# Kernel optimization log

Measured on AMD Instinct MI355X. Metric: run time of the kernel, lower is better.

Reference implementation:

```python
import jax, jax.numpy as jnp
import numpy as np

VOCAB, DIM, B, L, OUT = 100000, 50, 4096, 512, 20

def setup_inputs() -> dict:
    key = jax.random.key(0)
    k1, k2, k3, k4, k5 = jax.random.split(key, 5)
    x = jax.random.randint(k1, (B, L), 0, VOCAB, dtype=jnp.int64)
    lengths = jax.random.randint(k2, (B,), 1, L + 1, dtype=jnp.int64)  # at least 1 token
    emb_table = jax.random.normal(k3, (VOCAB, DIM), dtype=jnp.float32)
    W = jax.random.normal(k4, (OUT, DIM), dtype=jnp.float32) * 0.1
    b = jax.random.normal(k5, (OUT,), dtype=jnp.float32) * 0.1
    return {"x": x, "lengths": lengths, "emb_table": emb_table, "W": W, "b": b}

def reference(x, lengths, emb_table, W, b):
    # embedding gather: [B, L, D]
    emb = emb_table[x]
    # masked mean over the first lengths[i] tokens of each sample
    mask = (jnp.arange(emb.shape[1])[None, :] < lengths[:, None]).astype(emb.dtype)  # [B, L]
    denom = lengths.astype(emb.dtype)[:, None]                                        # [B, 1]
    rep = jnp.einsum('bld,bl->bd', emb, mask) / denom                                 # [B, D]
    rep = jax.nn.relu(rep)
    logits = rep @ W.T + b                                                            # [B, OUT]
    return logits
```

## Files before the change

kernel.cpp:

```cpp
#include <hip/hip_runtime.h>
#include <hip/hip_fp16.h>


#define LMAX    512
#define DIMV    50
#define OUTV    20
#define VOCABSZ 100000
#define RSTRIDE 64

struct __align__(16) H8 { __half2 h[4]; };

__global__ __launch_bounds__(256) void build_tab(
    const float* __restrict__ emb, __half* __restrict__ tab)
{
    const int t = blockIdx.x * 256 + threadIdx.x;
    const int r = t >> 3;
    const int q = t & 7;
    if (r > VOCABSZ) return;
    float v[8] = {0.f, 0.f, 0.f, 0.f, 0.f, 0.f, 0.f, 0.f};
    if (r < VOCABSZ) {
        const float* src = emb + r * DIMV + q * 8;
        if (q < 6) {
            #pragma unroll
            for (int j = 0; j < 8; j += 2) {
                float2 a = *reinterpret_cast<const float2*>(src + j);
                v[j] = a.x; v[j + 1] = a.y;
            }
        } else if (q == 6) {
            float2 a = *reinterpret_cast<const float2*>(src);
            v[0] = a.x; v[1] = a.y;
        }
    }
    H8 h;
    h.h[0] = __floats2half2_rn(v[0], v[1]);
    h.h[1] = __floats2half2_rn(v[2], v[3]);
    h.h[2] = __floats2half2_rn(v[4], v[5]);
    h.h[3] = __floats2half2_rn(v[6], v[7]);
    *reinterpret_cast<H8*>(tab + r * RSTRIDE + q * 8) = h;
}

__device__ inline void accum(float4& a0, float4& a1, const H8& h) {
    float2 f0 = __half22float2(h.h[0]);
    float2 f1 = __half22float2(h.h[1]);
    float2 f2 = __half22float2(h.h[2]);
    float2 f3 = __half22float2(h.h[3]);
    a0.x += f0.x; a0.y += f0.y; a0.z += f1.x; a0.w += f1.y;
    a1.x += f2.x; a1.y += f2.y; a1.z += f3.x; a1.w += f3.y;
}

__global__ __launch_bounds__(256) void fused_gather(
    const int*    __restrict__ x,
    const int*    __restrict__ lengths,
    const __half* __restrict__ tab,
    const float*  __restrict__ W,
    const float*  __restrict__ bias,
    float*        __restrict__ out)
{
    const int b    = blockIdx.x;
    const int tid  = threadIdx.x;
    const int wave = tid >> 6;
    const int lane = tid & 63;
    const int rg   = lane >> 3;
    const int cl   = lane & 7;

    __shared__ int   sidx[LMAX];
    __shared__ float sacc[4][64];
    __shared__ float srep[DIMV];

    const int len = lengths[b];

    const int xbase = b * LMAX;
    #pragma unroll
    for (int i = 0; i < LMAX; i += 256) {
        const int ii = i + tid;
        const int v  = x[xbase + ii];
        sidx[ii] = (ii < len) ? v : VOCABSZ;
    }
    __syncthreads();

    const __half* tabc = tab + cl * 8;
    const int nchunk = (len + 7) >> 3;
    float4 a0 = {0.f, 0.f, 0.f, 0.f};
    float4 a1 = {0.f, 0.f, 0.f, 0.f};

    int c = wave;
    for (; c + 28 < nchunk; c += 32) {
        int i0 = sidx[(c     ) * 8 + rg];
        int i1 = sidx[(c +  4) * 8 + rg];
        int i2 = sidx[(c +  8) * 8 + rg];
        int i3 = sidx[(c + 12) * 8 + rg];
        int i4 = sidx[(c + 16) * 8 + rg];
        int i5 = sidx[(c + 20) * 8 + rg];
        int i6 = sidx[(c + 24) * 8 + rg];
        int i7 = sidx[(c + 28) * 8 + rg];
        H8 h0 = *reinterpret_cast<const H8*>(tabc + (i0 << 6));
        H8 h1 = *reinterpret_cast<const H8*>(tabc + (i1 << 6));
        H8 h2 = *reinterpret_cast<const H8*>(tabc + (i2 << 6));
        H8 h3 = *reinterpret_cast<const H8*>(tabc + (i3 << 6));
        H8 h4 = *reinterpret_cast<const H8*>(tabc + (i4 << 6));
        H8 h5 = *reinterpret_cast<const H8*>(tabc + (i5 << 6));
        H8 h6 = *reinterpret_cast<const H8*>(tabc + (i6 << 6));
        H8 h7 = *reinterpret_cast<const H8*>(tabc + (i7 << 6));
        accum(a0, a1, h0); accum(a0, a1, h1); accum(a0, a1, h2); accum(a0, a1, h3);
        accum(a0, a1, h4); accum(a0, a1, h5); accum(a0, a1, h6); accum(a0, a1, h7);
    }
    for (; c < nchunk; c += 4) {
        int i0 = sidx[c * 8 + rg];
        H8 h0 = *reinterpret_cast<const H8*>(tabc + (i0 << 6));
        accum(a0, a1, h0);
    }

    #pragma unroll
    for (int m = 8; m <= 32; m <<= 1) {
        a0.x += __shfl_xor(a0.x, m); a0.y += __shfl_xor(a0.y, m);
        a0.z += __shfl_xor(a0.z, m); a0.w += __shfl_xor(a0.w, m);
        a1.x += __shfl_xor(a1.x, m); a1.y += __shfl_xor(a1.y, m);
        a1.z += __shfl_xor(a1.z, m); a1.w += __shfl_xor(a1.w, m);
    }
    if (lane < 8) {
        *reinterpret_cast<float4*>(&sacc[wave][lane * 8])     = a0;
        *reinterpret_cast<float4*>(&sacc[wave][lane * 8 + 4]) = a1;
    }
    __syncthreads();

    if (tid < DIMV) {
        float s = sacc[0][tid] + sacc[1][tid] + sacc[2][tid] + sacc[3][tid];
        srep[tid] = fmaxf(s / (float)len, 0.f);
    }
    __syncthreads();

    if (tid < OUTV) {
        float s = bias[tid];
        const float* wr = W + tid * DIMV;
        #pragma unroll
        for (int d = 0; d < DIMV; ++d) s += srep[d] * wr[d];
        out[b * OUTV + tid] = s;
    }
}

extern "C" void kernel_launch(void* const* d_in, const int* in_sizes, int n_in,
                              void* d_out, int out_size, void* d_ws, size_t ws_size,
                              hipStream_t stream) {
    const int*   x       = (const int*)  d_in[0];
    const int*   lengths = (const int*)  d_in[1];
    const float* emb     = (const float*)d_in[2];
    const float* W       = (const float*)d_in[3];
    const float* bias    = (const float*)d_in[4];
    float*  out = (float*)d_out;
    __half* tab = (__half*)d_ws;

    const int B = in_sizes[1];

    const int nthr = (VOCABSZ + 1) * 8;
    build_tab<<<(nthr + 255) / 256, 256, 0, stream>>>(emb, tab);
    fused_gather<<<B, 256, 0, stream>>>(x, lengths, tab, W, bias, out);
}
```

Measured before the change: 97.61 us.

## Bin token indices by vocab shard and gather per shard for cache locality

Merges table conversion with a per-sample binning pass that groups valid token indices into 8 vocabulary shards, padded to multiples of 8. A shard-major gather kernel then makes concurrently running blocks touch the same ~1.6MB slice of the half table, aiming to raise L2 hit rate, and writes per-shard partial sums. A finalize kernel reduces the partials and applies mean, ReLU and the linear layer. This adds an extra pass over the indices, workspace round trips and two more launches, and concurrently running blocks may not actually stay within one shard.

```diff
diff --git a/kernel.cpp b/kernel.cpp
--- a/kernel.cpp
+++ b/kernel.cpp
@@ -7,37 +7,16 @@
 #define OUTV    20
 #define VOCABSZ 100000
 #define RSTRIDE 64
+#define NSHARD  8
+#define SHROWS  12500
+#define BINCAP  576
+#define TABBLKS 3126
 
 struct __align__(16) H8 { __half2 h[4]; };
 
-__global__ __launch_bounds__(256) void build_tab(
-    const float* __restrict__ emb, __half* __restrict__ tab)
-{
-    const int t = blockIdx.x * 256 + threadIdx.x;
-    const int r = t >> 3;
-    const int q = t & 7;
-    if (r > VOCABSZ) return;
-    float v[8] = {0.f, 0.f, 0.f, 0.f, 0.f, 0.f, 0.f, 0.f};
-    if (r < VOCABSZ) {
-        const float* src = emb + r * DIMV + q * 8;
-        if (q < 6) {
-            #pragma unroll
-            for (int j = 0; j < 8; j += 2) {
-                float2 a = *reinterpret_cast<const float2*>(src + j);
-                v[j] = a.x; v[j + 1] = a.y;
-            }
-        } else if (q == 6) {
-            float2 a = *reinterpret_cast<const float2*>(src);
-            v[0] = a.x; v[1] = a.y;
-        }
-    }
-    H8 h;
-    h.h[0] = __floats2half2_rn(v[0], v[1]);
-    h.h[1] = __floats2half2_rn(v[2], v[3]);
-    h.h[2] = __floats2half2_rn(v[4], v[5]);
-    h.h[3] = __floats2half2_rn(v[6], v[7]);
-    *reinterpret_cast<H8*>(tab + r * RSTRIDE + q * 8) = h;
-}
+#define OFF_GBIN  (16u << 20)
+#define OFF_BOFS  (28u << 20)
+#define OFF_PART  (29u << 20)
 
 __device__ inline void accum(float4& a0, float4& a1, const H8& h) {
     float2 f0 = __half22float2(h.h[0]);
@@ -46,6 +25,174 @@
     float2 f3 = __half22float2(h.h[3]);
     a0.x += f0.x; a0.y += f0.y; a0.z += f1.x; a0.w += f1.y;
     a1.x += f2.x; a1.y += f2.y; a1.z += f3.x; a1.w += f3.y;
+}
+
+__global__ __launch_bounds__(256) void prep(
+    const float* __restrict__ emb, const int* __restrict__ x,
+    const int* __restrict__ lengths, char* __restrict__ ws)
+{
+    const int tid = threadIdx.x;
+
+    if (blockIdx.x < TABBLKS) {
+        __half* tab = (__half*)ws;
+        const int t = blockIdx.x * 256 + tid;
+        const int r = t >> 3, q = t & 7;
+        if (r > VOCABSZ) return;
+        float v[8] = {0.f,0.f,0.f,0.f,0.f,0.f,0.f,0.f};
+        if (r < VOCABSZ) {
+            const float* src = emb + r * DIMV + q * 8;
+            if (q < 6) {
+                #pragma unroll
+                for (int j = 0; j < 8; j += 2) {
+                    float2 a = *reinterpret_cast<const float2*>(src + j);
+                    v[j] = a.x; v[j + 1] = a.y;
+                }
+            } else if (q == 6) {
+                float2 a = *reinterpret_cast<const float2*>(src);
+                v[0] = a.x; v[1] = a.y;
+            }
+        }
+        H8 h;
+        h.h[0] = __floats2half2_rn(v[0], v[1]);
+        h.h[1] = __floats2half2_rn(v[2], v[3]);
+        h.h[2] = __floats2half2_rn(v[4], v[5]);
+        h.h[3] = __floats2half2_rn(v[6], v[7]);
+        *reinterpret_cast<H8*>(tab + r * RSTRIDE + q * 8) = h;
+        return;
+    }
+
+    const int b = blockIdx.x - TABBLKS;
+    int*  gbin = (int*)(ws + OFF_GBIN);
+    int2* bofs = (int2*)(ws + OFF_BOFS);
+
+    __shared__ int sidx[LMAX];
+    __shared__ int sbin[BINCAP];
+    __shared__ int cnt[NSHARD], pcnt[NSHARD], base[NSHARD], pos[NSHARD];
+
+    if (tid < NSHARD) { cnt[tid] = 0; pos[tid] = 0; }
+    __syncthreads();
+
+    const int len = lengths[b];
+    #pragma unroll
+    for (int i = tid; i < LMAX; i += 256) {
+        const int v = x[b * LMAX + i];
+        sidx[i] = v;
+        if (i < len) atomicAdd(&cnt[v / SHROWS], 1);
+    }
+    __syncthreads();
+    if (tid == 0) {
+        int run = 0;
+        #pragma unroll
+        for (int s = 0; s < NSHARD; ++s) {
+            base[s] = run;
+            pcnt[s] = (cnt[s] + 7) & ~7;
+            run += pcnt[s];
+        }
+    }
+    __syncthreads();
+    #pragma unroll
+    for (int i = tid; i < LMAX; i += 256) {
+        if (i < len) {
+            const int v = sidx[i];
+            const int s = v / SHROWS;
+            const int p = atomicAdd(&pos[s], 1);
+            sbin[base[s] + p] = v;
+        }
+    }
+    __syncthreads();
+    if (tid < 64) {
+        const int s = tid >> 3, k = tid & 7;
+        if (cnt[s] + k < pcnt[s]) sbin[base[s] + cnt[s] + k] = VOCABSZ;
+    }
+    __syncthreads();
+    const int total = base[NSHARD - 1] + pcnt[NSHARD - 1];
+    for (int j = tid; j < total; j += 256) gbin[b * BINCAP + j] = sbin[j];
+    if (tid < NSHARD) bofs[b * NSHARD + tid] = make_int2(base[tid], pcnt[tid]);
+}
+
+__global__ __launch_bounds__(256) void shard_gather(char* __restrict__ ws)
+{
+    const __half* tab  = (const __half*)ws;
+    const int*    gbin = (const int*)(ws + OFF_GBIN);
+    const int2*   bofs = (const int2*)(ws + OFF_BOFS);
+    float*        part = (float*)(ws + OFF_PART);
+
+    const int s    = blockIdx.x & 7;
+    const int grp  = blockIdx.x >> 3;
+    const int tid  = threadIdx.x;
+    const int wave = tid >> 6, lane = tid & 63;
+    const int rg   = lane >> 3, cl = lane & 7;
+    const int b    = grp * 4 + wave;
+
+    __shared__ int slab[4][520];
+
+    const int2 of = bofs[b * NSHARD + s];
+    const int* seg = gbin + b * BINCAP + of.x;
+    for (int i = lane; i < of.y; i += 64) slab[wave][i] = seg[i];
+    __syncthreads();
+
+    const __half* tabc = tab + cl * 8;
+    const int nch = of.y >> 3;
+    float4 a0 = {0.f,0.f,0.f,0.f}, a1 = {0.f,0.f,0.f,0.f};
+    int c = 0;
+    for (; c + 3 < nch; c += 4) {
+        const int i0 = slab[wave][(c    ) * 8 + rg];
+        const int i1 = slab[wave][(c + 1) * 8 + rg];
+        const int i2 = slab[wave][(c + 2) * 8 + rg];
+        const int i3 = slab[wave][(c + 3) * 8 + rg];
+        H8 h0 = *reinterpret_cast<const H8*>(tabc + (i0 << 6));
+        H8 h1 = *reinterpret_cast<const H8*>(tabc + (i1 << 6));
+        H8 h2 = *reinterpret_cast<const H8*>(tabc + (i2 << 6));
+        H8 h3 = *reinterpret_cast<const H8*>(tabc + (i3 << 6));
+        accum(a0, a1, h0); accum(a0, a1, h1);
+        accum(a0, a1, h2); accum(a0, a1, h3);
+    }
+    for (; c < nch; ++c) {
+        const int i0 = slab[wave][c * 8 + rg];
+        H8 h0 = *reinterpret_cast<const H8*>(tabc + (i0 << 6));
+        accum(a0, a1, h0);
+    }
+
+    #pragma unroll
+    for (int m = 8; m <= 32; m <<= 1) {
+        a0.x += __shfl_xor(a0.x, m); a0.y += __shfl_xor(a0.y, m);
+        a0.z += __shfl_xor(a0.z, m); a0.w += __shfl_xor(a0.w, m);
+        a1.x += __shfl_xor(a1.x, m); a1.y += __shfl_xor(a1.y, m);
+        a1.z += __shfl_xor(a1.z, m); a1.w += __shfl_xor(a1.w, m);
+    }
+    if (lane < 8) {
+        float* p = part + b * (NSHARD * 64) + s * 64 + lane * 8;
+        *reinterpret_cast<float4*>(p)     = a0;
+        *reinterpret_cast<float4*>(p + 4) = a1;
+    }
+}
+
+__global__ __launch_bounds__(256) void finalize(
+    const int* __restrict__ lengths, const float* __restrict__ W,
+    const float* __restrict__ bias, const char* __restrict__ ws,
+    float* __restrict__ out)
+{
+    const float* part = (const float*)(ws + OFF_PART);
+    const int tid = threadIdx.x, wave = tid >> 6, lane = tid & 63;
+    const int b = blockIdx.x * 4 + wave;
+
+    __shared__ float srep[4][64];
+
+    float v = 0.f;
+    #pragma unroll
+    for (int s = 0; s < NSHARD; ++s)
+        v += part[b * (NSHARD * 64) + s * 64 + lane];
+    const float inv = 1.0f / (float)lengths[b];
+    srep[wave][lane] = fmaxf(v * inv, 0.f);
+    __syncthreads();
+
+    if (lane < OUTV) {
+        float acc = bias[lane];
+        const float* wr = W + lane * DIMV;
+        #pragma unroll
+        for (int d = 0; d < DIMV; ++d) acc += srep[wave][d] * wr[d];
+        out[b * OUTV + lane] = acc;
+    }
 }
 
 __global__ __launch_bounds__(256) void fused_gather(
@@ -68,7 +215,6 @@
     __shared__ float srep[DIMV];
 
     const int len = lengths[b];
-
     const int xbase = b * LMAX;
     #pragma unroll
     for (int i = 0; i < LMAX; i += 256) {
@@ -80,8 +226,7 @@
 
     const __half* tabc = tab + cl * 8;
     const int nchunk = (len + 7) >> 3;
-    float4 a0 = {0.f, 0.f, 0.f, 0.f};
-    float4 a1 = {0.f, 0.f, 0.f, 0.f};
+    float4 a0 = {0.f,0.f,0.f,0.f}, a1 = {0.f,0.f,0.f,0.f};
 
     int c = wave;
     for (; c + 28 < nchunk; c += 32) {
@@ -146,12 +291,18 @@
     const float* emb     = (const float*)d_in[2];
     const float* W       = (const float*)d_in[3];
     const float* bias    = (const float*)d_in[4];
-    float*  out = (float*)d_out;
-    __half* tab = (__half*)d_ws;
+    float* out = (float*)d_out;
+    char*  ws  = (char*)d_ws;
 
     const int B = in_sizes[1];
-
-    const int nthr = (VOCABSZ + 1) * 8;
-    build_tab<<<(nthr + 255) / 256, 256, 0, stream>>>(emb, tab);
-    fused_gather<<<B, 256, 0, stream>>>(x, lengths, tab, W, bias, out);
-}
+    const size_t NEED = (size_t)OFF_PART + (size_t)B * NSHARD * 64 * sizeof(float);
+
+    if (ws_size >= NEED) {
+        prep<<<TABBLKS + B, 256, 0, stream>>>(emb, x, lengths, ws);
+        shard_gather<<<(B / 4) * NSHARD, 256, 0, stream>>>(ws);
+        finalize<<<B / 4, 256, 0, stream>>>(lengths, W, bias, ws, out);
+    } else {
+        prep<<<TABBLKS, 256, 0, stream>>>(emb, x, lengths, ws);
+        fused_gather<<<B, 256, 0, stream>>>(x, lengths, (const __half*)ws, W, bias, out);
+    }
+}
```

Result: slower. 103.4 us (+6.0%).
